# Kernel tuning notes

Measured on AMD Instinct MI355X. Metric: run time of the kernel, lower is better.

## Reference

```python
import jax, jax.numpy as jnp
import numpy as np

B, T, D = 4, 2048, 1024

def layer_norm(x, gamma, bias):
    # NOTE: faithfully reproduces the source's (buggy) LN: x - mu/sqrt(var), unbiased var
    mu = jnp.mean(x, axis=-1, keepdims=True)
    var = jnp.var(x, axis=-1, ddof=1, keepdims=True)
    return (x - mu / jnp.sqrt(var)) * gamma + bias

def setup_inputs() -> dict:
    key = jax.random.key(0)
    ks = jax.random.split(key, 8)
    scale = 1.0 / np.sqrt(D)
    return {
        'x': jax.random.normal(ks[0], (B, T, D), dtype=jnp.float32),
        'gamma1': jnp.ones((D,), jnp.float32),
        'beta1': jnp.zeros((D,), jnp.float32),
        'w_q': jax.random.uniform(ks[1], (D, D), jnp.float32, -scale, scale),
        'w_k': jax.random.uniform(ks[2], (D, D), jnp.float32, -scale, scale),
        'w_v': jax.random.uniform(ks[3], (D, D), jnp.float32, -scale, scale),
        'gamma2': jnp.ones((D,), jnp.float32),
        'beta2': jnp.zeros((D,), jnp.float32),
        'W1': jax.random.uniform(ks[4], (D, D), jnp.float32, -scale, scale),
        'b1': jnp.zeros((D,), jnp.float32),
        'W2': jax.random.uniform(ks[5], (D, D), jnp.float32, -scale, scale),
        'b2': jnp.zeros((D,), jnp.float32),
    }

def reference(x, gamma1, beta1, w_q, w_k, w_v, gamma2, beta2, W1, b1, W2, b2):
    d_model = x.shape[-1]
    t = x.shape[1]
    h = layer_norm(x, gamma1, beta1)
    q = jnp.einsum('btk,kd->btd', h, w_q)
    k = jnp.einsum('btk,kd->btd', h, w_k)
    v = jnp.einsum('btk,kd->btd', h, w_v)
    scale = 1.0 / jnp.sqrt(jnp.asarray(d_model, x.dtype))
    causal = jnp.tril(jnp.ones((t, t), dtype=bool))
    mask = jnp.where(causal, 0.0, -jnp.inf).astype(x.dtype)
    scores = jnp.einsum('bqd,bkd->bqk', q, k) * scale + mask
    attn = jax.nn.softmax(scores, axis=-1)
    y = jnp.einsum('bqt,btd->bqd', attn, v) + x
    h2 = layer_norm(y, gamma2, beta2)
    out = jnp.maximum(h2 @ W1 + b1, 0.0) @ W2 + b2
    return out + y
```

## Files before the change

kernel.cpp:

```cpp
#include <hip/hip_runtime.h>
#include <hip/hip_bf16.h>
#include <math.h>

using bf16 = __hip_bfloat16;

static constexpr int Bn = 4;
static constexpr int Tn = 2048;
static constexpr int Dn = 1024;

typedef __attribute__((ext_vector_type(8))) short bf16x8;
typedef __attribute__((ext_vector_type(4))) float f32x4;

__device__ __forceinline__ float ldf(float v) { return v; }
__device__ __forceinline__ float ldf(bf16 v) { return __bfloat162float(v); }
__device__ __forceinline__ bf16 f2b(float v) { return __float2bfloat16(v); }
__device__ __forceinline__ float b2f(short s) {
    return __uint_as_float(((unsigned)(unsigned short)s) << 16);
}
__device__ __forceinline__ short f2bs(float v) {
    bf16 t = __float2bfloat16(v);
    return *reinterpret_cast<short*>(&t);
}

template <typename T> __device__ __forceinline__ T from_float(float v);
template <> __device__ __forceinline__ float from_float<float>(float v) { return v; }
template <> __device__ __forceinline__ bf16 from_float<bf16>(float v) { return f2b(v); }

__device__ __forceinline__ void load4(const float* p, float* v) {
    const float4 t = *(const float4*)p;
    v[0] = t.x; v[1] = t.y; v[2] = t.z; v[3] = t.w;
}
__device__ __forceinline__ void load4(const bf16* p, float* v) {
    const short4 t = *(const short4*)p;
    v[0] = b2f(t.x); v[1] = b2f(t.y); v[2] = b2f(t.z); v[3] = b2f(t.w);
}

__device__ __forceinline__ void async_copy16(const bf16* g, bf16* l) {
    __builtin_amdgcn_global_load_lds(
        (const __attribute__((address_space(1))) void*)g,
        (__attribute__((address_space(3))) void*)l,
        16, 0, 0);
}


template <int BN, int EPI, int MODE, typename OutT>
__global__ __launch_bounds__(512, 2) void gemm8p(
    const bf16* __restrict__ A, const bf16* __restrict__ Bm,
    OutT* __restrict__ C, float* __restrict__ c2,
    const float* __restrict__ bias, const bf16* __restrict__ res,
    bf16* __restrict__ vtp, float* __restrict__ rowsum,
    int K, int lda, int ldb, int ldc, long sA, long sB, long sC)
{
    static_assert(EPI != 1 || BN == 128, "V-transpose epilogue needs BN=128");
    constexpr int BM = 256, BK = 32;
    constexpr int NT = BN / 64;
    constexpr int BUFE = (BM + BN) * BK;
    __shared__ __align__(16) bf16 smem[3 * BUFE];

    int bm, bn, bz = 0, chunk = 0;
    if constexpr (MODE == 1) {
        bn = blockIdx.x; bz = blockIdx.y; bm = blockIdx.z;
        if (bn > bm) return;
    } else if constexpr (MODE == 2) {
        bn = blockIdx.x; bz = blockIdx.y;
        const int zc = blockIdx.z;
        bm = 7 - (zc >> 1);
        chunk = zc & 1;
    } else {
        bm = blockIdx.x; bn = blockIdx.y; bz = blockIdx.z;
    }

    int kbeg = 0, kmax = K;
    if constexpr (MODE == 2) {
        const int keff = (bm + 1) * BM;
        const int half = keff >> 1;
        kbeg = chunk ? half : 0;
        kmax = chunk ? keff : half;
    }
    const int NK = (kmax - kbeg) >> 5;

    const bf16* Ab = A + (size_t)bz * sA;
    const bf16* Bb = Bm + (size_t)bz * sB;

    const int tid = threadIdx.x;
    const int wave = tid >> 6;
    const int lane = tid & 63;
    const int wm = wave >> 2;
    const int wn = wave & 3;
    const int lr = lane >> 2;
    const int lc = ((lane & 3) ^ ((lane >> 5) << 1)) * 8;
    const int arow = lane & 15;
    const int kq = ((lane >> 4) * 8) ^ ((lane & 8) << 1);

    const bf16* gA0 = Ab + (size_t)(bm * BM + wave * 16 + lr) * lda + lc + kbeg;
    const bf16* gA1 = Ab + (size_t)(bm * BM + (wave + 8) * 16 + lr) * lda + lc + kbeg;
    const bf16* gB0 = Bb + (size_t)(bn * BN + wave * 16 + lr) * ldb + lc + kbeg;
    const bf16* gB1 = (BN == 256)
        ? Bb + (size_t)(bn * BN + (wave + 8) * 16 + lr) * ldb + lc + kbeg : nullptr;

    f32x4 acc[8][NT] = {};

    {
        bf16* As0 = smem;
        bf16* Bs0 = smem + BM * BK;
        bf16* As1 = smem + BUFE;
        bf16* Bs1 = smem + BUFE + BM * BK;
        async_copy16(gA0, As0 + wave * 512);
        async_copy16(gA1, As0 + (wave + 8) * 512);
        async_copy16(gB0, Bs0 + wave * 512);
        if constexpr (BN == 256) async_copy16(gB1, Bs0 + (wave + 8) * 512);
        async_copy16(gA0 + BK, As1 + wave * 512);
        async_copy16(gA1 + BK, As1 + (wave + 8) * 512);
        async_copy16(gB0 + BK, Bs1 + wave * 512);
        if constexpr (BN == 256) async_copy16(gB1 + BK, Bs1 + (wave + 8) * 512);
    }
    if constexpr (BN == 256) asm volatile("s_waitcnt vmcnt(4)" ::: "memory");
    else                     asm volatile("s_waitcnt vmcnt(3)" ::: "memory");
    __builtin_amdgcn_s_barrier();

    int cb = 0;
    int sb = 2;
    for (int kt = 0; kt < NK; ++kt) {
        const bf16* As = smem + cb * BUFE;
        const bf16* Bs = As + BM * BK;
        const bool st = (kt + 2) < NK;
        const int koff = (kt + 2) * BK;

        bf16x8 af[8], bf0[NT / 2];
#pragma unroll
        for (int mt = 0; mt < 8; ++mt)
            af[mt] = *(const bf16x8*)&As[(wm * 8 + mt) * 512 + arow * 32 + kq];
#pragma unroll
        for (int nt = 0; nt < NT / 2; ++nt)
            bf0[nt] = *(const bf16x8*)&Bs[(wn * NT + nt) * 512 + arow * 32 + kq];
        if (st) {
            bf16* Ad = smem + sb * BUFE;
            async_copy16(gA0 + koff, Ad + wave * 512);
            async_copy16(gA1 + koff, Ad + (wave + 8) * 512);
        }
        __builtin_amdgcn_s_barrier();
        asm volatile("s_waitcnt lgkmcnt(0)" ::: "memory");
        __builtin_amdgcn_sched_barrier(0);
        __builtin_amdgcn_s_setprio(1);
#pragma unroll
        for (int mt = 0; mt < 8; ++mt)
#pragma unroll
            for (int nt = 0; nt < NT / 2; ++nt)
                acc[mt][nt] = __builtin_amdgcn_mfma_f32_16x16x32_bf16(
                    af[mt], bf0[nt], acc[mt][nt], 0, 0, 0);
        __builtin_amdgcn_s_setprio(0);
        __builtin_amdgcn_s_barrier();

        bf16x8 bf1[NT / 2];
#pragma unroll
        for (int nt = 0; nt < NT / 2; ++nt)
            bf1[nt] = *(const bf16x8*)&Bs[(wn * NT + NT / 2 + nt) * 512 + arow * 32 + kq];
        if (st) {
            bf16* Bd = smem + sb * BUFE + BM * BK;
            async_copy16(gB0 + koff, Bd + wave * 512);
            if constexpr (BN == 256) async_copy16(gB1 + koff, Bd + (wave + 8) * 512);
        }
        __builtin_amdgcn_s_barrier();
        asm volatile("s_waitcnt lgkmcnt(0)" ::: "memory");
        __builtin_amdgcn_sched_barrier(0);
        __builtin_amdgcn_s_setprio(1);
#pragma unroll
        for (int mt = 0; mt < 8; ++mt)
#pragma unroll
            for (int nt = 0; nt < NT / 2; ++nt)
                acc[mt][NT / 2 + nt] = __builtin_amdgcn_mfma_f32_16x16x32_bf16(
                    af[mt], bf1[nt], acc[mt][NT / 2 + nt], 0, 0, 0);
        __builtin_amdgcn_s_setprio(0);
        if (st) {
            if constexpr (BN == 256) asm volatile("s_waitcnt vmcnt(4)" ::: "memory");
            else                     asm volatile("s_waitcnt vmcnt(3)" ::: "memory");
        } else {
            asm volatile("s_waitcnt vmcnt(0)" ::: "memory");
        }
        __builtin_amdgcn_s_barrier();

        cb = (cb + 1 == 3) ? 0 : cb + 1;
        sb = (sb + 1 == 3) ? 0 : sb + 1;
    }

    const int qrow = (lane >> 4) * 4;
    const int ccol = lane & 15;
    const int row0 = bm * BM + wm * 128;
    const int col0 = bn * BN + wn * (NT * 16);

    if constexpr (EPI == 1) {
        bf16* tt = smem;
#pragma unroll
        for (int mt = 0; mt < 8; ++mt)
#pragma unroll
            for (int nt = 0; nt < NT; ++nt) {
                const int dl = wn * (NT * 16) + nt * 16 + ccol;
                const int tl = wm * 128 + mt * 16 + qrow;
                short4 o;
                o.x = f2bs(acc[mt][nt][0]);
                o.y = f2bs(acc[mt][nt][1]);
                o.z = f2bs(acc[mt][nt][2]);
                o.w = f2bs(acc[mt][nt][3]);
                *(short4*)&tt[dl * 264 + tl] = o;
            }
        __syncthreads();
        const int b = (bm * BM) >> 11;
        const int tin = (bm * BM) & (Tn - 1);
        const int dr = tid >> 4;
        const int t0 = (tid & 15) * 16;
#pragma unroll
        for (int p = 0; p < 4; ++p) {
            const int d = p * 32 + dr;
            const bf16* srcl = &tt[d * 264 + t0];
            bf16* dst = vtp + ((size_t)b * Dn + bn * BN + d) * Tn + tin + t0;
            ((bf16x8*)dst)[0] = ((const bf16x8*)srcl)[0];
            ((bf16x8*)dst)[1] = ((const bf16x8*)srcl)[1];
        }
        return;
    }

    if constexpr (EPI == 2) {
        OutT* Cb = C + (size_t)bz * sC;
        float* rsb = rowsum + (size_t)bz * Tn;
        const float scale = 0.03125f;
#pragma unroll
        for (int mt = 0; mt < 8; ++mt) {
            float rsv[4] = {0.f, 0.f, 0.f, 0.f};
#pragma unroll
            for (int nt = 0; nt < NT; ++nt) {
                const int cc = col0 + nt * 16 + ccol;
#pragma unroll
                for (int r = 0; r < 4; ++r) {
                    const int rr = row0 + mt * 16 + qrow + r;
                    float e = 0.0f;
                    if (cc <= rr) {
                        const short es = f2bs(__expf(acc[mt][nt][r] * scale));
                        Cb[(size_t)rr * ldc + cc] = *(const bf16*)&es;
                        e = b2f(es);
                    } else {
                        Cb[(size_t)rr * ldc + cc] = from_float<OutT>(0.0f);
                    }
                    rsv[r] += e;
                }
            }
#pragma unroll
            for (int r = 0; r < 4; ++r) {
                float v = rsv[r];
                v += __shfl_xor(v, 1);
                v += __shfl_xor(v, 2);
                v += __shfl_xor(v, 4);
                v += __shfl_xor(v, 8);
                if (ccol == 0)
                    atomicAdd(rsb + row0 + mt * 16 + qrow + r, v);
            }
        }
        return;
    }

    if constexpr (EPI == 3) {
        float* Cb = (chunk ? c2 : (float*)C) + (size_t)bz * sC;
#pragma unroll
        for (int mt = 0; mt < 8; ++mt)
#pragma unroll
            for (int nt = 0; nt < NT; ++nt) {
                const int cc = col0 + nt * 16 + ccol;
#pragma unroll
                for (int r = 0; r < 4; ++r) {
                    const int rr = row0 + mt * 16 + qrow + r;
                    Cb[(size_t)rr * ldc + cc] = acc[mt][nt][r];
                }
            }
        return;
    }

#pragma unroll
    for (int mt = 0; mt < 8; ++mt)
#pragma unroll
        for (int nt = 0; nt < NT; ++nt) {
            const int cc = col0 + nt * 16 + ccol;
            const float bv = bias ? bias[cc] : 0.0f;
#pragma unroll
            for (int r = 0; r < 4; ++r) {
                const int rr = row0 + mt * 16 + qrow + r;
                float v = acc[mt][nt][r] + bv;
                if (res) v += b2f(*(const short*)&res[(size_t)rr * ldc + cc]);
                C[(size_t)rr * ldc + cc] = from_float<OutT>(v);
            }
        }
}

template <int BM, int BN, int MINW, int EPI, typename OutT, typename ResT, bool RELU>
__global__ __launch_bounds__(256, MINW) void gemm_nt(
    const bf16* __restrict__ A, const bf16* __restrict__ Bm,
    OutT* __restrict__ C, const float* __restrict__ bias,
    const ResT* __restrict__ res,
    int M, int N, int K, int lda, int ldb, int ldc)
{
    const int bm = blockIdx.x, bn = blockIdx.y;

    constexpr int WROWS = BM / 64;
    constexpr int WCOLS = 4 / WROWS;
    constexpr int TM = 64;
    constexpr int TN = BN / WCOLS;
    constexpr int MT = TM / 16;
    constexpr int NT = TN / 16;
    constexpr int nA = BM / 16;
    constexpr int nB = BN / 16;
    constexpr int STAGE = 2 * (BM + BN) * 32;

    __shared__ __align__(16) bf16 smem[STAGE];
    bf16* As = smem;
    bf16* Bs = smem + 2 * BM * 32;

    const int tid = threadIdx.x;
    const int wave = tid >> 6;
    const int lane = tid & 63;
    const int wm = wave / WCOLS;
    const int wn = wave % WCOLS;

    f32x4 acc[MT][NT] = {};

    const int lr = lane >> 2;
    const int lc = ((lane & 3) ^ ((lane >> 5) << 1)) * 8;
    const bf16* gAc[nA / 4]; bf16* lAc[nA / 4];
    const bf16* gBc[nB / 4]; bf16* lBc[nB / 4];
#pragma unroll
    for (int i = 0; i < nA / 4; ++i) {
        const int c = wave + 4 * i;
        gAc[i] = A + (size_t)(bm * BM + c * 16 + lr) * lda + lc;
        lAc[i] = &As[c * 512];
    }
#pragma unroll
    for (int i = 0; i < nB / 4; ++i) {
        const int c = wave + 4 * i;
        gBc[i] = Bm + (size_t)(bn * BN + c * 16 + lr) * ldb + lc;
        lBc[i] = &Bs[c * 512];
    }

    const int arow = lane & 15;
    const int kq = ((lane >> 4) * 8) ^ ((lane & 8) << 1);

    for (int k0 = 0; k0 < K; k0 += 64) {
#pragma unroll
        for (int hh = 0; hh < 2; ++hh) {
#pragma unroll
            for (int i = 0; i < nA / 4; ++i)
                async_copy16(gAc[i] + k0 + 32 * hh, lAc[i] + hh * (BM * 32));
#pragma unroll
            for (int i = 0; i < nB / 4; ++i)
                async_copy16(gBc[i] + k0 + 32 * hh, lBc[i] + hh * (BN * 32));
        }
        __syncthreads();

#pragma unroll
        for (int hh = 0; hh < 2; ++hh) {
            const bf16* Ah = As + hh * (BM * 32);
            const bf16* Bh = Bs + hh * (BN * 32);
            bf16x8 af[MT], bfm[NT];
#pragma unroll
            for (int t = 0; t < MT; ++t)
                af[t] = *(const bf16x8*)&Ah[(wm * TM + t * 16 + arow) * 32 + kq];
#pragma unroll
            for (int t = 0; t < NT; ++t)
                bfm[t] = *(const bf16x8*)&Bh[(wn * TN + t * 16 + arow) * 32 + kq];
#pragma unroll
            for (int mt = 0; mt < MT; ++mt)
#pragma unroll
                for (int nt = 0; nt < NT; ++nt)
                    acc[mt][nt] = __builtin_amdgcn_mfma_f32_16x16x32_bf16(
                        af[mt], bfm[nt], acc[mt][nt], 0, 0, 0);
        }
        __syncthreads();
    }

    const int rowBase = bm * BM + wm * TM;
    const int colBase = bn * BN + wn * TN;
    const int qrow = (lane >> 4) * 4;
    const int ccol = lane & 15;

#pragma unroll
    for (int mt = 0; mt < MT; ++mt) {
#pragma unroll
        for (int nt = 0; nt < NT; ++nt) {
            const int cc = colBase + nt * 16 + ccol;
            const float bv = bias ? bias[cc] : 0.0f;
#pragma unroll
            for (int r = 0; r < 4; ++r) {
                const int rr = rowBase + mt * 16 + qrow + r;
                float v = acc[mt][nt][r] + bv;
                if (RELU) v = fmaxf(v, 0.0f);
                if (res) v += ldf(res[(size_t)rr * ldc + cc]);
                C[(size_t)rr * ldc + cc] = from_float<OutT>(v);
            }
        }
    }
}

template <typename InT>
__device__ __forceinline__ void ln_row(
    const InT* __restrict__ xr, const float* __restrict__ gamma,
    const float* __restrict__ beta, bf16* __restrict__ orow, int tid)
{
    const int j = tid * 4;
    float v[4];
    load4(xr + j, v);
    float s = v[0] + v[1] + v[2] + v[3];
    float sq = v[0] * v[0] + v[1] * v[1] + v[2] * v[2] + v[3] * v[3];
#pragma unroll
    for (int o = 32; o > 0; o >>= 1) {
        s += __shfl_down(s, o);
        sq += __shfl_down(sq, o);
    }
    __shared__ float red[2][4];
    const int lane = tid & 63, w = tid >> 6;
    if (lane == 0) { red[0][w] = s; red[1][w] = sq; }
    __syncthreads();
    s  = red[0][0] + red[0][1] + red[0][2] + red[0][3];
    sq = red[1][0] + red[1][1] + red[1][2] + red[1][3];
    const float mean = s / (float)Dn;
    const float var = (sq - s * s / (float)Dn) / (float)(Dn - 1);
    const float coef = mean * rsqrtf(var);

    const float4 g = *(const float4*)(gamma + j);
    const float4 be = *(const float4*)(beta + j);
    short4 o;
    o.x = f2bs((v[0] - coef) * g.x + be.x);
    o.y = f2bs((v[1] - coef) * g.y + be.y);
    o.z = f2bs((v[2] - coef) * g.z + be.z);
    o.w = f2bs((v[3] - coef) * g.w + be.w);
    *(short4*)(orow + j) = o;
}

__global__ __launch_bounds__(256) void ln2_fused(
    const float* __restrict__ yp0, const float* __restrict__ yp1,
    const float* __restrict__ rowsum, const float* __restrict__ x,
    const float* __restrict__ gamma, const float* __restrict__ beta,
    bf16* __restrict__ y, bf16* __restrict__ h2)
{
    const int row = blockIdx.x;
    const int tid = threadIdx.x;
    const int j = tid * 4;
    const size_t base = (size_t)row * Dn;
    const float inv = 1.0f / rowsum[row];

    float p0[4], p1[4], xv[4], v[4];
    load4(yp0 + base + j, p0);
    load4(yp1 + base + j, p1);
    load4(x + base + j, xv);
    short4 yo;
    v[0] = (p0[0] + p1[0]) * inv + xv[0];
    v[1] = (p0[1] + p1[1]) * inv + xv[1];
    v[2] = (p0[2] + p1[2]) * inv + xv[2];
    v[3] = (p0[3] + p1[3]) * inv + xv[3];
    yo.x = f2bs(v[0]); yo.y = f2bs(v[1]); yo.z = f2bs(v[2]); yo.w = f2bs(v[3]);
    *(short4*)(y + base + j) = yo;

    float s = v[0] + v[1] + v[2] + v[3];
    float sq = v[0] * v[0] + v[1] * v[1] + v[2] * v[2] + v[3] * v[3];
#pragma unroll
    for (int o = 32; o > 0; o >>= 1) {
        s += __shfl_down(s, o);
        sq += __shfl_down(sq, o);
    }
    __shared__ float red[2][4];
    const int lane = tid & 63, w = tid >> 6;
    if (lane == 0) { red[0][w] = s; red[1][w] = sq; }
    __syncthreads();
    s  = red[0][0] + red[0][1] + red[0][2] + red[0][3];
    sq = red[1][0] + red[1][1] + red[1][2] + red[1][3];
    const float mean = s / (float)Dn;
    const float var = (sq - s * s / (float)Dn) / (float)(Dn - 1);
    const float coef = mean * rsqrtf(var);

    const float4 g = *(const float4*)(gamma + j);
    const float4 be = *(const float4*)(beta + j);
    short4 o;
    o.x = f2bs((v[0] - coef) * g.x + be.x);
    o.y = f2bs((v[1] - coef) * g.y + be.y);
    o.z = f2bs((v[2] - coef) * g.z + be.z);
    o.w = f2bs((v[3] - coef) * g.w + be.w);
    *(short4*)(h2 + base + j) = o;
}

struct WPtrs { const float* p[5]; };

__global__ __launch_bounds__(256) void prep_kernel(
    WPtrs wp, bf16* __restrict__ wdst, float* __restrict__ rowsum,
    const float* __restrict__ x, const float* __restrict__ gamma1,
    const float* __restrict__ beta1, bf16* __restrict__ h)
{
    const int bx = blockIdx.x;
    if (bx < 5120) {
        __shared__ bf16 tile[32][33];
        const int z = bx >> 10;
        const int t = bx & 1023;
        const float* src = wp.p[z];
        bf16* d = wdst + (size_t)z * Dn * Dn;
        const int c0 = (t & 31) * 32, r0 = (t >> 5) * 32;
        const int tx = threadIdx.x & 31;
        const int ty = threadIdx.x >> 5;
#pragma unroll
        for (int dy = 0; dy < 32; dy += 8)
            tile[ty + dy][tx] = f2b(src[(size_t)(r0 + ty + dy) * Dn + (c0 + tx)]);
        __syncthreads();
#pragma unroll
        for (int dy = 0; dy < 32; dy += 8)
            d[(size_t)(c0 + ty + dy) * Dn + (r0 + tx)] = tile[tx][ty + dy];
    } else if (bx < 5128) {
        const int base = (bx - 5120) * 1024;
#pragma unroll
        for (int i = 0; i < 4; ++i) rowsum[base + i * 256 + threadIdx.x] = 0.0f;
    } else {
        const int row = bx - 5128;
        ln_row(x + (size_t)row * Dn, gamma1, beta1, h + (size_t)row * Dn, threadIdx.x);
    }
}

extern "C" void kernel_launch(void* const* d_in, const int* in_sizes, int n_in,
                              void* d_out, int out_size, void* d_ws, size_t ws_size,
                              hipStream_t stream) {
    const float* x      = (const float*)d_in[0];
    const float* gamma1 = (const float*)d_in[1];
    const float* beta1  = (const float*)d_in[2];
    const float* w_q    = (const float*)d_in[3];
    const float* w_k    = (const float*)d_in[4];
    const float* w_v    = (const float*)d_in[5];
    const float* gamma2 = (const float*)d_in[6];
    const float* beta2  = (const float*)d_in[7];
    const float* W1     = (const float*)d_in[8];
    const float* b1     = (const float*)d_in[9];
    const float* W2     = (const float*)d_in[10];
    const float* b2     = (const float*)d_in[11];
    float* out = (float*)d_out;

    char* ws = (char*)d_ws;
    size_t off = 0;
    auto alloc = [&](size_t bytes) {
        char* p = ws + off;
        off += (bytes + 255) & ~(size_t)255;
        return p;
    };
    const size_t BT = (size_t)Bn * Tn;
    bf16* h    = (bf16*)alloc(BT * Dn * 2);
    bf16* qk   = (bf16*)alloc(BT * 2 * Dn * 2);
    bf16* vt   = (bf16*)alloc(BT * Dn * 2);
    bf16* wbuf = (bf16*)alloc((size_t)5 * Dn * Dn * 2);
    bf16* S    = (bf16*)alloc((size_t)Bn * Tn * Tn * 2);
    bf16* y    = (bf16*)alloc(BT * Dn * 2);
    float* rowsum = (float*)alloc((size_t)Bn * Tn * 4);
    float* yp1 = (float*)alloc(BT * Dn * 4);
    float* yp0 = (float*)qk;
    bf16* h2   = h;
    bf16* mid  = qk;

    const dim3 blk(256);
    const dim3 blk512(512);
    const long TD  = (long)Tn * Dn;
    const long TT  = (long)Tn * Tn;
    const long TD2 = (long)Tn * 2 * Dn;
    const size_t DD = (size_t)Dn * Dn;

    WPtrs wp; wp.p[0] = w_q; wp.p[1] = w_k; wp.p[2] = w_v; wp.p[3] = W1; wp.p[4] = W2;
    prep_kernel<<<dim3(5128 + (unsigned)BT, 1, 1), blk, 0, stream>>>(
        wp, wbuf, rowsum, x, gamma1, beta1, h);

    gemm8p<256, 0, 0, bf16><<<dim3(32, 8, 1), blk512, 0, stream>>>(
        h, wbuf, qk, nullptr, nullptr, nullptr, nullptr, nullptr,
        Dn, Dn, Dn, 2 * Dn, 0, 0, 0);

    gemm8p<128, 1, 0, bf16><<<dim3(32, 8, 1), blk512, 0, stream>>>(
        h, wbuf + 2 * DD, (bf16*)nullptr, nullptr, nullptr, nullptr, vt, nullptr,
        Dn, Dn, Dn, 0, 0, 0, 0);

    gemm8p<256, 2, 1, bf16><<<dim3(8, Bn, 8), blk512, 0, stream>>>(
        qk, qk + 1024, S, nullptr, nullptr, nullptr, nullptr, rowsum,
        Dn, 2 * Dn, 2 * Dn, Tn, TD2, TD2, TT);

    gemm8p<256, 3, 2, float><<<dim3(4, Bn, 16), blk512, 0, stream>>>(
        S, vt, yp0, yp1, nullptr, nullptr, nullptr, nullptr,
        Tn, Tn, Tn, Dn, TT, TD, TD);

    ln2_fused<<<dim3((unsigned)BT), blk, 0, stream>>>(
        yp0, yp1, rowsum, x, gamma2, beta2, y, h2);

    gemm_nt<128, 128, 4, 0, bf16, float, true><<<dim3(64, 8, 1), blk, 0, stream>>>(
        h2, wbuf + 3 * DD, mid, b1, nullptr,
        (int)BT, Dn, Dn, Dn, Dn, Dn);

    gemm_nt<128, 128, 4, 0, float, bf16, false><<<dim3(64, 8, 1), blk, 0, stream>>>(
        mid, wbuf + 4 * DD, out, b2, y,
        (int)BT, Dn, Dn, Dn, Dn, Dn);
}
```

Measured before the change: 337.6 us.

## Rebalance split-K work in PV GEMM via lookup table and store bf16 partials

The causal P·V GEMM previously split each row-block's K range into two equal halves, so work per block varied widely across row blocks. A constant lookup table now maps the 16 z-indices to (row block, chunk, K range) so that per-block work is roughly equal, with up to three chunks for the larger row blocks. Partial outputs are stored as bf16 instead of fp32, and the LN2 kernel sums one to three partials depending on the row block. This cuts write and read traffic and reduces tail imbalance, at the cost of some extra rounding in the partial sums.

```diff
diff --git a/kernel.cpp b/kernel.cpp
--- a/kernel.cpp
+++ b/kernel.cpp
@@ -42,6 +42,11 @@
         16, 0, 0);
 }
 
+
+__device__ __constant__ int zbm_t[16] = {7,7,5,5,4,4,6,6,6,7,3,3,1,2,2,0};
+__device__ __constant__ int zj_t [16] = {0,1,0,1,0,1,0,1,2,2,0,1,0,0,1,0};
+__device__ __constant__ int zk0_t[16] = {0,12,0,12,0,10,0,10,19,24,0,8,0,0,6,0};
+__device__ __constant__ int zk1_t[16] = {12,24,12,24,10,20,10,19,28,32,8,16,8,6,12,4};
 
 template <int BN, int EPI, int MODE, typename OutT>
 __global__ __launch_bounds__(512, 2) void gemm8p(
@@ -58,24 +63,19 @@
     __shared__ __align__(16) bf16 smem[3 * BUFE];
 
     int bm, bn, bz = 0, chunk = 0;
+    int kbeg = 0, kmax = K;
     if constexpr (MODE == 1) {
         bn = blockIdx.x; bz = blockIdx.y; bm = blockIdx.z;
         if (bn > bm) return;
     } else if constexpr (MODE == 2) {
         bn = blockIdx.x; bz = blockIdx.y;
         const int zc = blockIdx.z;
-        bm = 7 - (zc >> 1);
-        chunk = zc & 1;
+        bm = zbm_t[zc];
+        chunk = zj_t[zc];
+        kbeg = zk0_t[zc] * 64;
+        kmax = zk1_t[zc] * 64;
     } else {
         bm = blockIdx.x; bn = blockIdx.y; bz = blockIdx.z;
-    }
-
-    int kbeg = 0, kmax = K;
-    if constexpr (MODE == 2) {
-        const int keff = (bm + 1) * BM;
-        const int half = keff >> 1;
-        kbeg = chunk ? half : 0;
-        kmax = chunk ? keff : half;
     }
     const int NK = (kmax - kbeg) >> 5;
 
@@ -258,7 +258,11 @@
     }
 
     if constexpr (EPI == 3) {
-        float* Cb = (chunk ? c2 : (float*)C) + (size_t)bz * sC;
+        bf16* Cb;
+        if (chunk == 0)      Cb = (bf16*)C;
+        else if (chunk == 1) Cb = (bf16*)c2;
+        else                 Cb = vtp;
+        Cb += (size_t)bz * sC;
 #pragma unroll
         for (int mt = 0; mt < 8; ++mt)
 #pragma unroll
@@ -267,7 +271,7 @@
 #pragma unroll
                 for (int r = 0; r < 4; ++r) {
                     const int rr = row0 + mt * 16 + qrow + r;
-                    Cb[(size_t)rr * ldc + cc] = acc[mt][nt][r];
+                    Cb[(size_t)rr * ldc + cc] = f2b(acc[mt][nt][r]);
                 }
             }
         return;
@@ -432,7 +436,8 @@
 }
 
 __global__ __launch_bounds__(256) void ln2_fused(
-    const float* __restrict__ yp0, const float* __restrict__ yp1,
+    const bf16* __restrict__ yp0, const bf16* __restrict__ yp1,
+    const bf16* __restrict__ yp2,
     const float* __restrict__ rowsum, const float* __restrict__ x,
     const float* __restrict__ gamma, const float* __restrict__ beta,
     bf16* __restrict__ y, bf16* __restrict__ h2)
@@ -443,15 +448,27 @@
     const size_t base = (size_t)row * Dn;
     const float inv = 1.0f / rowsum[row];
 
-    float p0[4], p1[4], xv[4], v[4];
-    load4(yp0 + base + j, p0);
-    load4(yp1 + base + j, p1);
+    const int bmrow = (row & (Tn - 1)) >> 8;
+    const int nch = (bmrow < 2) ? 1 : (bmrow < 6 ? 2 : 3);
+
+    float p[4], xv[4], v[4];
+    load4(yp0 + base + j, p);
+    if (nch > 1) {
+        float q[4];
+        load4(yp1 + base + j, q);
+        p[0] += q[0]; p[1] += q[1]; p[2] += q[2]; p[3] += q[3];
+    }
+    if (nch > 2) {
+        float q[4];
+        load4(yp2 + base + j, q);
+        p[0] += q[0]; p[1] += q[1]; p[2] += q[2]; p[3] += q[3];
+    }
     load4(x + base + j, xv);
     short4 yo;
-    v[0] = (p0[0] + p1[0]) * inv + xv[0];
-    v[1] = (p0[1] + p1[1]) * inv + xv[1];
-    v[2] = (p0[2] + p1[2]) * inv + xv[2];
-    v[3] = (p0[3] + p1[3]) * inv + xv[3];
+    v[0] = p[0] * inv + xv[0];
+    v[1] = p[1] * inv + xv[1];
+    v[2] = p[2] * inv + xv[2];
+    v[3] = p[3] * inv + xv[3];
     yo.x = f2bs(v[0]); yo.y = f2bs(v[1]); yo.z = f2bs(v[2]); yo.w = f2bs(v[3]);
     *(short4*)(y + base + j) = yo;
 
@@ -548,8 +565,10 @@
     bf16* S    = (bf16*)alloc((size_t)Bn * Tn * Tn * 2);
     bf16* y    = (bf16*)alloc(BT * Dn * 2);
     float* rowsum = (float*)alloc((size_t)Bn * Tn * 4);
-    float* yp1 = (float*)alloc(BT * Dn * 4);
-    float* yp0 = (float*)qk;
+    bf16* yp12 = (bf16*)alloc(BT * Dn * 2 * 2);
+    bf16* yp0 = (bf16*)qk;
+    bf16* yp1 = yp12;
+    bf16* yp2 = yp12 + BT * Dn;
     bf16* h2   = h;
     bf16* mid  = qk;
 
@@ -576,12 +595,12 @@
         qk, qk + 1024, S, nullptr, nullptr, nullptr, nullptr, rowsum,
         Dn, 2 * Dn, 2 * Dn, Tn, TD2, TD2, TT);
 
-    gemm8p<256, 3, 2, float><<<dim3(4, Bn, 16), blk512, 0, stream>>>(
-        S, vt, yp0, yp1, nullptr, nullptr, nullptr, nullptr,
+    gemm8p<256, 3, 2, bf16><<<dim3(4, Bn, 16), blk512, 0, stream>>>(
+        S, vt, yp0, (float*)yp1, nullptr, nullptr, yp2, nullptr,
         Tn, Tn, Tn, Dn, TT, TD, TD);
 
     ln2_fused<<<dim3((unsigned)BT), blk, 0, stream>>>(
-        yp0, yp1, rowsum, x, gamma2, beta2, y, h2);
+        yp0, yp1, yp2, rowsum, x, gamma2, beta2, y, h2);
 
     gemm_nt<128, 128, 4, 0, bf16, float, true><<<dim3(64, 8, 1), blk, 0, stream>>>(
         h2, wbuf + 3 * DD, mid, b1, nullptr,
```

Result: no change. 333.3 us (-1.3%).
